# Optimization experiments

Measured on AMD Instinct MI355X. Metric: run time of the kernel, lower is better.

The kernel has to match this reference:

```python
import jax, jax.numpy as jnp
import numpy as np

B, C, H, W = 8, 3, 768, 1024
SAMPLE_RATIO = 0.15
G = int(H * W * SAMPLE_RATIO)  # 117964 point triplets
DELTA_COS = 0.867
DELTA_DIFF = 0.005  # hardcoded in select_points_groups' filter_mask call
DELTA_Z = 1e-4


def setup_inputs() -> dict:
    key = jax.random.key(0)
    ks = jax.random.split(key, 8)
    gt = jax.random.normal(ks[0], (B, C, H, W), dtype=jnp.float32)
    pred = jax.random.normal(ks[1], (B, C, H, W), dtype=jnp.float32)
    idx = {}
    for i, (nm, hi) in enumerate([("p1_x", W), ("p1_y", H), ("p2_x", W),
                                  ("p2_y", H), ("p3_x", W), ("p3_y", H)]):
        idx[nm] = jax.random.randint(ks[2 + i], (G,), 0, hi, dtype=jnp.int32)
    return {"gt": gt, "pred": pred, **idx}


def _form_groups(pw, p1_x, p1_y, p2_x, p2_y, p3_x, p3_y):
    # pw: [B,H,W,3] -> groups [B,G,3coord,3pts]
    g1 = pw[:, p1_y, p1_x, :]
    g2 = pw[:, p2_y, p2_x, :]
    g3 = pw[:, p3_y, p3_x, :]
    return jnp.stack([g1, g2, g3], axis=3)


def _vn_loss(gt, pred, p1_x, p1_y, p2_x, p2_y, p3_x, p3_y):
    pw_gt = jnp.transpose(gt, (0, 2, 3, 1))    # [B,H,W,3]
    pw_pred = jnp.transpose(pred, (0, 2, 3, 1))

    pw_g = _form_groups(pw_gt, p1_x, p1_y, p2_x, p2_y, p3_x, p3_y)  # [B,G,3,3]

    # pairwise difference vectors: 12, 13, 23 -> [B,G,3coord,3pair]
    pw12 = pw_g[..., 1] - pw_g[..., 0]
    pw13 = pw_g[..., 2] - pw_g[..., 0]
    pw23 = pw_g[..., 2] - pw_g[..., 1]
    pw_diff = jnp.stack([pw12, pw13, pw23], axis=3)

    # cosine-similarity (Gram) filter: energy[b,g,i,j] = <diff_i, diff_j>
    energy = jnp.einsum("bgci,bgcj->bgij", pw_diff, pw_diff)
    norms = jnp.sqrt(jnp.sum(pw_diff * pw_diff, axis=2))  # [B,G,3]
    nm = norms[..., :, None] * norms[..., None, :]
    norm_energy = energy / (nm + 1e-8)
    mask_cos = jnp.sum((norm_energy > DELTA_COS) | (norm_energy < -DELTA_COS),
                       axis=(2, 3)) > 3                   # [B,G]

    mask_pad = jnp.sum(pw_g[:, :, 2, :] > DELTA_Z, axis=2) == 3
    mask_x = jnp.sum(jnp.abs(pw_diff[:, :, 0, :]) < DELTA_DIFF, axis=2) > 0
    mask_y = jnp.sum(jnp.abs(pw_diff[:, :, 1, :]) < DELTA_DIFF, axis=2) > 0
    mask_z = jnp.sum(jnp.abs(pw_diff[:, :, 2, :]) < DELTA_DIFF, axis=2) > 0
    mask = mask_pad & ~((mask_x & mask_y & mask_z) | mask_cos)  # [B,G]

    pw_gp = _form_groups(pw_pred, p1_x, p1_y, p2_x, p2_y, p3_x, p3_y)
    # torch quirk: boolean mask over [B,G,3] (z of each point) indexes the
    # first 3 dims [B,G,coord], zeroing whole coord-rows to 1e-4
    zmask = pw_gp[:, :, 2, :] == 0.0
    pw_gp = jnp.where(zmask[:, :, :, None], 1e-4, pw_gp)

    def normals(groups):
        p12 = groups[..., 1] - groups[..., 0]
        p13 = groups[..., 2] - groups[..., 0]
        n = jnp.cross(p12, p13, axis=2)
        norm = jnp.linalg.norm(n, axis=2, keepdims=True)
        norm = norm + jnp.where(norm == 0.0, 0.01, 0.0)
        return n / norm

    gt_n = normals(pw_g)
    dt_n = normals(pw_gp)

    per_group = jnp.sum(jnp.abs(gt_n - dt_n), axis=2)  # [B,G]
    m = mask.astype(per_group.dtype)
    # mean over selected groups (batch dims flattened by the torch reshape)
    return jnp.sum(per_group * m) / jnp.maximum(jnp.sum(m), 1.0)


def reference(gt, pred, p1_x, p1_y, p2_x, p2_y, p3_x, p3_y):
    return _vn_loss(gt, pred, p1_x, p1_y, p2_x, p2_y, p3_x, p3_y)
```

## Files before the change

kernel.cpp:

```cpp
#include <hip/hip_runtime.h>
#include <hip/hip_fp16.h>

#define HW_ (768 * 1024)
#define W_ 1024
#define DC 0.867f
#define DD 0.005f
#define DZ 0.0001f

#define SEG_STRIDE 130

__device__ __forceinline__ void vn_group_math(
    const float G1[3], const float G2[3], const float G3[3],
    const float P1[3], const float P2[3], const float P3[3],
    float& s_loss, float& s_cnt)
{
    float d0[3], d1[3], d2[3];
    #pragma unroll
    for (int c = 0; c < 3; c++) {
        d0[c] = G2[c] - G1[c];
        d1[c] = G3[c] - G1[c];
        d2[c] = G3[c] - G2[c];
    }

    float e00 = d0[0]*d0[0] + d0[1]*d0[1] + d0[2]*d0[2];
    float e11 = d1[0]*d1[0] + d1[1]*d1[1] + d1[2]*d1[2];
    float e22 = d2[0]*d2[0] + d2[1]*d2[1] + d2[2]*d2[2];
    float e01 = d0[0]*d1[0] + d0[1]*d1[1] + d0[2]*d1[2];
    float e02 = d0[0]*d2[0] + d0[1]*d2[1] + d0[2]*d2[2];
    float e12 = d1[0]*d2[0] + d1[1]*d2[1] + d1[2]*d2[2];
    float s0 = sqrtf(e00), s1 = sqrtf(e11), s2 = sqrtf(e22);

    int cc = 0;
    {
        float ne;
        ne = e00 / (s0*s0 + 1e-8f); cc += (ne > DC) || (ne < -DC);
        ne = e11 / (s1*s1 + 1e-8f); cc += (ne > DC) || (ne < -DC);
        ne = e22 / (s2*s2 + 1e-8f); cc += (ne > DC) || (ne < -DC);
        ne = e01 / (s0*s1 + 1e-8f); cc += 2 * ((ne > DC) || (ne < -DC));
        ne = e02 / (s0*s2 + 1e-8f); cc += 2 * ((ne > DC) || (ne < -DC));
        ne = e12 / (s1*s2 + 1e-8f); cc += 2 * ((ne > DC) || (ne < -DC));
    }
    bool mask_cos = cc > 3;
    bool mask_pad = (G1[2] > DZ) && (G2[2] > DZ) && (G3[2] > DZ);
    bool mx = (fabsf(d0[0]) < DD) || (fabsf(d1[0]) < DD) || (fabsf(d2[0]) < DD);
    bool my = (fabsf(d0[1]) < DD) || (fabsf(d1[1]) < DD) || (fabsf(d2[1]) < DD);
    bool mz = (fabsf(d0[2]) < DD) || (fabsf(d1[2]) < DD) || (fabsf(d2[2]) < DD);
    bool mask = mask_pad && !((mx && my && mz) || mask_cos);

    if (mask) {
        float n0 = d0[1]*d1[2] - d0[2]*d1[1];
        float n1 = d0[2]*d1[0] - d0[0]*d1[2];
        float n2 = d0[0]*d1[1] - d0[1]*d1[0];
        float nn = sqrtf(n0*n0 + n1*n1 + n2*n2);
        if (nn == 0.f) nn = 0.01f;

        bool zm[3] = { P1[2] == 0.f, P2[2] == 0.f, P3[2] == 0.f };
        float Q1[3], Q2[3], Q3[3];
        #pragma unroll
        for (int c = 0; c < 3; c++) {
            Q1[c] = zm[c] ? 0.0001f : P1[c];
            Q2[c] = zm[c] ? 0.0001f : P2[c];
            Q3[c] = zm[c] ? 0.0001f : P3[c];
        }
        float q0[3], q1[3];
        #pragma unroll
        for (int c = 0; c < 3; c++) {
            q0[c] = Q2[c] - Q1[c];
            q1[c] = Q3[c] - Q1[c];
        }
        float m0 = q0[1]*q1[2] - q0[2]*q1[1];
        float m1 = q0[2]*q1[0] - q0[0]*q1[2];
        float m2 = q0[0]*q1[1] - q0[1]*q1[0];
        float mn = sqrtf(m0*m0 + m1*m1 + m2*m2);
        if (mn == 0.f) mn = 0.01f;

        s_loss += fabsf(n0/nn - m0/mn) + fabsf(n1/nn - m1/mn) + fabsf(n2/nn - m2/mn);
        s_cnt  += 1.f;
    }
}

__device__ __forceinline__ void vn_reduce_store(float s_loss, float s_cnt, double* acc)
{
    #pragma unroll
    for (int off = 32; off > 0; off >>= 1) {
        s_loss += __shfl_down(s_loss, off);
        s_cnt  += __shfl_down(s_cnt,  off);
    }
    __shared__ float ls[4], lc[4];
    int lane = threadIdx.x & 63;
    int wid  = threadIdx.x >> 6;
    if (lane == 0) { ls[wid] = s_loss; lc[wid] = s_cnt; }
    __syncthreads();
    if (threadIdx.x == 0) {
        float tl = ls[0] + ls[1] + ls[2] + ls[3];
        float tc = lc[0] + lc[1] + lc[2] + lc[3];
        atomicAdd(acc,     (double)tl);
        atomicAdd(acc + 1, (double)tc);
    }
}

__global__ __launch_bounds__(256) void vn_pack_t(
    const float* __restrict__ gt, const float* __restrict__ pred,
    uint4* __restrict__ rec)
{
    __shared__ __half lh[48 * SEG_STRIDE];

    size_t px_base = (size_t)blockIdx.x * 128;
    int t = threadIdx.x;
    int w = t >> 6, l = t & 63;

    float2 v[12];
    #pragma unroll
    for (int k = 0; k < 12; k++) {
        int s = w * 12 + k;
        int b = s / 6, c = s % 6;
        const float* src = (c < 3)
            ? gt   + ((size_t)b * 3 + c)       * HW_ + px_base
            : pred + ((size_t)b * 3 + (c - 3)) * HW_ + px_base;
        v[k] = *(const float2*)(src + l * 2);
    }
    #pragma unroll
    for (int k = 0; k < 12; k++) {
        int s = w * 12 + k;
        __half2 h2 = __floats2half2_rn(v[k].x, v[k].y);
        *(unsigned int*)(&lh[s * SEG_STRIDE + l * 2]) = *(unsigned int*)&h2;
    }

    __syncthreads();

    int b  = t & 7;
    int c6 = b * 6;
    uint4* out = rec + px_base * 8;
    #pragma unroll
    for (int r = 0; r < 4; r++) {
        int j    = t + r * 256;
        int i_px = j >> 3;
        uint4 o;
        __half2* hh = (__half2*)&o;
        hh[0] = __halves2half2(lh[(c6 + 0) * SEG_STRIDE + i_px],
                               lh[(c6 + 1) * SEG_STRIDE + i_px]);
        hh[1] = __halves2half2(lh[(c6 + 2) * SEG_STRIDE + i_px],
                               lh[(c6 + 3) * SEG_STRIDE + i_px]);
        hh[2] = __halves2half2(lh[(c6 + 4) * SEG_STRIDE + i_px],
                               lh[(c6 + 5) * SEG_STRIDE + i_px]);
        o.w = 0u;
        out[j] = o;
    }
}

__device__ __forceinline__ void unpack_rec(uint4 r, float G[3], float P[3])
{
    __half2 a = *(__half2*)&r.x;
    __half2 b = *(__half2*)&r.y;
    __half2 c = *(__half2*)&r.z;
    G[0] = __low2float(a);  G[1] = __high2float(a);
    G[2] = __low2float(b);  P[0] = __high2float(b);
    P[1] = __low2float(c);  P[2] = __high2float(c);
}

__global__ __launch_bounds__(256) void vn_gather_h(
    const uint4* __restrict__ rec,
    const int* __restrict__ p1x, const int* __restrict__ p1y,
    const int* __restrict__ p2x, const int* __restrict__ p2y,
    const int* __restrict__ p3x, const int* __restrict__ p3y,
    int G, double* __restrict__ acc)
{
    int t = blockIdx.x * 256 + threadIdx.x;
    int g = t >> 1;
    int h = (t & 1) * 4;

    float s_loss = 0.f, s_cnt = 0.f;

    if (g < G) {
        size_t q1 = ((size_t)(p1y[g] * W_ + p1x[g])) * 8 + h;
        size_t q2 = ((size_t)(p2y[g] * W_ + p2x[g])) * 8 + h;
        size_t q3 = ((size_t)(p3y[g] * W_ + p3x[g])) * 8 + h;

        uint4 r1[4], r2[4], r3[4];
        #pragma unroll
        for (int j = 0; j < 4; j++) r1[j] = rec[q1 + j];
        #pragma unroll
        for (int j = 0; j < 4; j++) r2[j] = rec[q2 + j];
        #pragma unroll
        for (int j = 0; j < 4; j++) r3[j] = rec[q3 + j];

        #pragma unroll
        for (int j = 0; j < 4; j++) {
            float G1[3], P1[3], G2[3], P2[3], G3[3], P3[3];
            unpack_rec(r1[j], G1, P1);
            unpack_rec(r2[j], G2, P2);
            unpack_rec(r3[j], G3, P3);
            vn_group_math(G1, G2, G3, P1, P2, P3, s_loss, s_cnt);
        }
    }

    vn_reduce_store(s_loss, s_cnt, acc);
}

__global__ __launch_bounds__(256) void vn_main(
    const float* __restrict__ gt, const float* __restrict__ pred,
    const int* __restrict__ p1x, const int* __restrict__ p1y,
    const int* __restrict__ p2x, const int* __restrict__ p2y,
    const int* __restrict__ p3x, const int* __restrict__ p3y,
    int G, double* __restrict__ acc)
{
    int g = blockIdx.x * 256 + threadIdx.x;
    int b = blockIdx.y;

    float s_loss = 0.f, s_cnt = 0.f;

    if (g < G) {
        int o1 = p1y[g] * W_ + p1x[g];
        int o2 = p2y[g] * W_ + p2x[g];
        int o3 = p3y[g] * W_ + p3x[g];
        const float* gb = gt   + (size_t)b * 3 * HW_;
        const float* pb = pred + (size_t)b * 3 * HW_;

        float G1[3], G2[3], G3[3], P1[3], P2[3], P3[3];
        #pragma unroll
        for (int c = 0; c < 3; c++) {
            G1[c] = gb[c * HW_ + o1];
            G2[c] = gb[c * HW_ + o2];
            G3[c] = gb[c * HW_ + o3];
            P1[c] = pb[c * HW_ + o1];
            P2[c] = pb[c * HW_ + o2];
            P3[c] = pb[c * HW_ + o3];
        }
        vn_group_math(G1, G2, G3, P1, P2, P3, s_loss, s_cnt);
    }

    vn_reduce_store(s_loss, s_cnt, acc);
}

__global__ void vn_final(const double* __restrict__ acc, float* __restrict__ out)
{
    float s = (float)acc[0];
    float c = (float)acc[1];
    out[0] = s / fmaxf(c, 1.0f);
}

extern "C" void kernel_launch(void* const* d_in, const int* in_sizes, int n_in,
                              void* d_out, int out_size, void* d_ws, size_t ws_size,
                              hipStream_t stream) {
    const float* gt   = (const float*)d_in[0];
    const float* pred = (const float*)d_in[1];
    const int* p1x = (const int*)d_in[2];
    const int* p1y = (const int*)d_in[3];
    const int* p2x = (const int*)d_in[4];
    const int* p2y = (const int*)d_in[5];
    const int* p3x = (const int*)d_in[6];
    const int* p3y = (const int*)d_in[7];

    int G = in_sizes[2];
    int B = in_sizes[0] / (3 * HW_);
    double* acc = (double*)d_ws;

    hipMemsetAsync(acc, 0, 2 * sizeof(double), stream);

    size_t rec_bytes = (size_t)HW_ * 8 * sizeof(uint4);
    size_t need = 256 + rec_bytes;

    if (B == 8 && ws_size >= need) {
        uint4* rec = (uint4*)((char*)d_ws + 256);
        vn_pack_t<<<HW_ / 128, 256, 0, stream>>>(gt, pred, rec);
        int nthreads = G * 2;
        vn_gather_h<<<(nthreads + 255) / 256, 256, 0, stream>>>(
            rec, p1x, p1y, p2x, p2y, p3x, p3y, G, acc);
    } else {
        dim3 grid((G + 255) / 256, B);
        vn_main<<<grid, 256, 0, stream>>>(gt, pred, p1x, p1y, p2x, p2y, p3x, p3y, G, acc);
    }

    vn_final<<<1, 1, 0, stream>>>(acc, (float*)d_out);
}
```

Measured before the change: 79.73 us.

## Mark sampled pixels and pack only touched pixel records

A new kernel sets a per-pixel bitmask from the sampled triplet indices using atomicOr. The pack kernel then writes the interleaved half-precision record only for pixels that some triplet actually references. With random sampling only a minority of pixels are touched, so this aims to cut most of the large write traffic into the record buffer. The cost is an extra memset and a small kernel launch, plus a branch in the store loop. The load loop is also merged with the convert-and-store loop, which may reduce how many loads are in flight at once.

```diff
diff --git a/kernel.cpp b/kernel.cpp
--- a/kernel.cpp
+++ b/kernel.cpp
@@ -99,17 +99,35 @@
     }
 }
 
-__global__ __launch_bounds__(256) void vn_pack_t(
+__global__ __launch_bounds__(256) void vn_mark(
+    const int* __restrict__ p1x, const int* __restrict__ p1y,
+    const int* __restrict__ p2x, const int* __restrict__ p2y,
+    const int* __restrict__ p3x, const int* __restrict__ p3y,
+    int G, unsigned int* __restrict__ mask)
+{
+    int g = blockIdx.x * 256 + threadIdx.x;
+    if (g >= G) return;
+    int a = p1y[g] * W_ + p1x[g];
+    int b = p2y[g] * W_ + p2x[g];
+    int c = p3y[g] * W_ + p3x[g];
+    atomicOr(&mask[a >> 5], 1u << (a & 31));
+    atomicOr(&mask[b >> 5], 1u << (b & 31));
+    atomicOr(&mask[c >> 5], 1u << (c & 31));
+}
+
+__global__ __launch_bounds__(256) void vn_pack_m(
     const float* __restrict__ gt, const float* __restrict__ pred,
-    uint4* __restrict__ rec)
+    const unsigned int* __restrict__ mask, uint4* __restrict__ rec)
 {
     __shared__ __half lh[48 * SEG_STRIDE];
+    __shared__ unsigned int lmask[4];
 
     size_t px_base = (size_t)blockIdx.x * 128;
     int t = threadIdx.x;
     int w = t >> 6, l = t & 63;
 
-    float2 v[12];
+    if (t < 4) lmask[t] = mask[(px_base >> 5) + t];
+
     #pragma unroll
     for (int k = 0; k < 12; k++) {
         int s = w * 12 + k;
@@ -117,12 +135,8 @@
         const float* src = (c < 3)
             ? gt   + ((size_t)b * 3 + c)       * HW_ + px_base
             : pred + ((size_t)b * 3 + (c - 3)) * HW_ + px_base;
-        v[k] = *(const float2*)(src + l * 2);
-    }
-    #pragma unroll
-    for (int k = 0; k < 12; k++) {
-        int s = w * 12 + k;
-        __half2 h2 = __floats2half2_rn(v[k].x, v[k].y);
+        float2 v = *(const float2*)(src + l * 2);
+        __half2 h2 = __floats2half2_rn(v.x, v.y);
         *(unsigned int*)(&lh[s * SEG_STRIDE + l * 2]) = *(unsigned int*)&h2;
     }
 
@@ -135,16 +149,19 @@
     for (int r = 0; r < 4; r++) {
         int j    = t + r * 256;
         int i_px = j >> 3;
-        uint4 o;
-        __half2* hh = (__half2*)&o;
-        hh[0] = __halves2half2(lh[(c6 + 0) * SEG_STRIDE + i_px],
-                               lh[(c6 + 1) * SEG_STRIDE + i_px]);
-        hh[1] = __halves2half2(lh[(c6 + 2) * SEG_STRIDE + i_px],
-                               lh[(c6 + 3) * SEG_STRIDE + i_px]);
-        hh[2] = __halves2half2(lh[(c6 + 4) * SEG_STRIDE + i_px],
-                               lh[(c6 + 5) * SEG_STRIDE + i_px]);
-        o.w = 0u;
-        out[j] = o;
+        bool touched = (lmask[i_px >> 5] >> (i_px & 31)) & 1u;
+        if (touched) {
+            uint4 o;
+            __half2* hh = (__half2*)&o;
+            hh[0] = __halves2half2(lh[(c6 + 0) * SEG_STRIDE + i_px],
+                                   lh[(c6 + 1) * SEG_STRIDE + i_px]);
+            hh[1] = __halves2half2(lh[(c6 + 2) * SEG_STRIDE + i_px],
+                                   lh[(c6 + 3) * SEG_STRIDE + i_px]);
+            hh[2] = __halves2half2(lh[(c6 + 4) * SEG_STRIDE + i_px],
+                                   lh[(c6 + 5) * SEG_STRIDE + i_px]);
+            o.w = 0u;
+            out[j] = o;
+        }
     }
 }
 
@@ -257,12 +274,19 @@
 
     hipMemsetAsync(acc, 0, 2 * sizeof(double), stream);
 
-    size_t rec_bytes = (size_t)HW_ * 8 * sizeof(uint4);
-    size_t need = 256 + rec_bytes;
+    size_t mask_off   = 256;
+    size_t mask_bytes = (HW_ / 32) * sizeof(unsigned int);
+    size_t rec_off    = 131072;
+    size_t rec_bytes  = (size_t)HW_ * 8 * sizeof(uint4);
+    size_t need = rec_off + rec_bytes;
 
     if (B == 8 && ws_size >= need) {
-        uint4* rec = (uint4*)((char*)d_ws + 256);
-        vn_pack_t<<<HW_ / 128, 256, 0, stream>>>(gt, pred, rec);
+        unsigned int* mask = (unsigned int*)((char*)d_ws + mask_off);
+        uint4*        rec  = (uint4*)((char*)d_ws + rec_off);
+
+        hipMemsetAsync(mask, 0, mask_bytes, stream);
+        vn_mark<<<(G + 255) / 256, 256, 0, stream>>>(p1x, p1y, p2x, p2y, p3x, p3y, G, mask);
+        vn_pack_m<<<HW_ / 128, 256, 0, stream>>>(gt, pred, mask, rec);
         int nthreads = G * 2;
         vn_gather_h<<<(nthreads + 255) / 256, 256, 0, stream>>>(
             rec, p1x, p1y, p2x, p2y, p3x, p3y, G, acc);
```

Result: slower. 90.19 us (+13.1%).
